# Kernel optimization log

Measured on AMD Instinct MI355X. Metric: run time of the kernel, lower is better.

Reference implementation:

```python
import jax, jax.numpy as jnp
import numpy as np

B, L, D, R = 16, 256, 1024, 128

def setup_inputs() -> dict:
    key = jax.random.key(0)
    k1, k2 = jax.random.split(key)
    batch = jax.random.normal(k1, (B, L, D), dtype=jnp.float32)
    # proj initialized uniform(-0.05, 0.05) in the original
    proj = jax.random.uniform(k2, (D, R), dtype=jnp.float32, minval=-0.05, maxval=0.05)
    return {"batch": batch, "proj": proj}

def reference(batch, proj):
    # [B, L, R] projected embeddings
    t = jnp.matmul(batch, proj)
    # all-pairs squared L2 distances: sum_r (t[b,i,r] - t[b,j,r])^2 -> [B, L, L]
    diffs = t[:, :, None, :] - t[:, None, :, :]  # [B, L, L, R]
    squared_distances = jnp.sum(diffs * diffs, axis=-1)
    return squared_distances
```

## Files before the change

### kernel.cpp

```cpp
#include <hip/hip_runtime.h>
#include <stdint.h>

#define B_ 16
#define L_ 256
#define D_ 1024
#define R_ 128
#define M_ (B_*L_)

typedef short short8 __attribute__((ext_vector_type(8)));
typedef float f32x4 __attribute__((ext_vector_type(4)));

__device__ __forceinline__ unsigned short f2bf(float f) {
  union { float f; unsigned int u; } v; v.f = f;
  unsigned int r = v.u + 0x7FFFu + ((v.u >> 16) & 1u);
  return (unsigned short)(r >> 16);
}
__device__ __forceinline__ float bf2f(unsigned short s) {
  union { unsigned int u; float f; } v; v.u = ((unsigned int)s) << 16;
  return v.f;
}
__device__ __forceinline__ void gload_lds16(const void* g, void* l) {
  __builtin_amdgcn_global_load_lds(
      (const __attribute__((address_space(1))) unsigned int*)g,
      (__attribute__((address_space(3))) unsigned int*)l, 16, 0, 0);
}

__global__ __launch_bounds__(256) void k0_transpose_cast(
    const float* __restrict__ P, unsigned short* __restrict__ PbT) {
  int id = blockIdx.x * 256 + threadIdx.x;
  int n  = id & 127;
  int kc = id >> 7;
  union { unsigned short s[8]; uint4 v; } u;
#pragma unroll
  for (int j = 0; j < 8; ++j) u.s[j] = f2bf(P[(kc * 8 + j) * R_ + n]);
  *reinterpret_cast<uint4*>(&PbT[(size_t)n * D_ + kc * 8]) = u.v;
}

__global__ __launch_bounds__(512) void k1_gemm(
    const float* __restrict__ X, const unsigned short* __restrict__ PbT,
    unsigned short* __restrict__ Tb, float* __restrict__ Nrm) {
  __shared__ unsigned short sX[2][16 * 128];
  __shared__ unsigned short sP[2][128 * 128];
  __shared__ float nacc[16][8];

  const int tid  = threadIdx.x;
  const int lane = tid & 63;
  const int w    = tid >> 6;
  const int m0   = blockIdx.x * 16;

  const int xr = tid >> 5;
  const int xk = (tid & 31) * 4;

  f32x4 acc;
  acc[0] = 0.f; acc[1] = 0.f; acc[2] = 0.f; acc[3] = 0.f;

  auto stage = [&](int buf, int kt) {
    const int k0 = kt * 128;
    float4 xv = *reinterpret_cast<const float4*>(&X[(size_t)(m0 + xr) * D_ + k0 + xk]);
    uint2 p;
    p.x = (unsigned int)f2bf(xv.x) | ((unsigned int)f2bf(xv.y) << 16);
    p.y = (unsigned int)f2bf(xv.z) | ((unsigned int)f2bf(xv.w) << 16);
    int byte_in_row = (xk * 2) ^ ((xr & 7) << 4);
    *reinterpret_cast<uint2*>(reinterpret_cast<char*>(&sX[buf][0]) + xr * 256 + byte_in_row) = p;
#pragma unroll
    for (int i = 0; i < 4; ++i) {
      int c = tid + 512 * i;
      int row = c >> 4, ch = c & 15;
      gload_lds16(&PbT[(size_t)row * D_ + k0 + ((ch ^ (row & 7)) * 8)],
                  reinterpret_cast<char*>(&sP[buf][0]) + c * 16);
    }
  };

  auto compute = [&](int buf) {
    const char* xb = reinterpret_cast<const char*>(&sX[buf][0]);
    const char* pb = reinterpret_cast<const char*>(&sP[buf][0]);
    const int nb = w * 16;
#pragma unroll
    for (int s = 0; s < 4; ++s) {
      int koffb = s * 64 + ((lane >> 4) << 4);
      int ar = lane & 15;
      short8 a = *reinterpret_cast<const short8*>(xb + ar * 256 + (koffb ^ ((ar & 7) << 4)));
      int br = nb + (lane & 15);
      short8 b = *reinterpret_cast<const short8*>(pb + br * 256 + (koffb ^ ((br & 7) << 4)));
      acc = __builtin_amdgcn_mfma_f32_16x16x32_bf16(a, b, acc, 0, 0, 0);
    }
  };

  stage(0, 0);
  __syncthreads();
  int buf = 0;
#pragma unroll
  for (int kt = 0; kt < 8; ++kt) {
    if (kt < 7) stage(buf ^ 1, kt + 1);
    compute(buf);
    __syncthreads();
    buf ^= 1;
  }

  const int nb = w * 16;
  const int col = lane & 15;
#pragma unroll
  for (int q = 0; q < 4; ++q) {
    int row = ((lane >> 4) << 2) + q;
    unsigned short hv = f2bf(acc[q]);
    Tb[(size_t)(m0 + row) * R_ + nb + col] = hv;
    float tr = bf2f(hv);
    float s = tr * tr;
    s += __shfl_xor(s, 1); s += __shfl_xor(s, 2);
    s += __shfl_xor(s, 4); s += __shfl_xor(s, 8);
    if (col == 0) nacc[row][w] = s;
  }
  __syncthreads();
  if (tid < 16) {
    float t = 0.f;
#pragma unroll
    for (int i = 0; i < 8; ++i) t += nacc[tid][i];
    Nrm[m0 + tid] = t;
  }
}

__global__ __launch_bounds__(256) void k2_gram(
    const unsigned short* __restrict__ Tb, const float* __restrict__ Nrm,
    float* __restrict__ Out) {
  __shared__ unsigned short sI[2 * 16 * 64];
  __shared__ unsigned short sJ[2 * 128 * 64];

  const int tid  = threadIdx.x;
  const int lane = tid & 63;
  const int w    = tid >> 6;
  const int blk  = blockIdx.x;
  const int b    = blk >> 5;
  const int it   = (blk >> 1) & 15;
  const int jh   = blk & 1;

  {
    int h = tid >> 7, row = (tid >> 3) & 15, ch = tid & 7;
    gload_lds16(&Tb[(size_t)(b * L_ + it * 16 + row) * R_ + h * 64 + ((ch ^ (row & 7)) * 8)],
                reinterpret_cast<char*>(sI) + tid * 16);
  }
#pragma unroll
  for (int i = 0; i < 8; ++i) {
    int c = tid + 256 * i;
    int h = c >> 10, row = (c >> 3) & 127, ch = c & 7;
    gload_lds16(&Tb[(size_t)(b * L_ + jh * 128 + row) * R_ + h * 64 + ((ch ^ (row & 7)) * 8)],
                reinterpret_cast<char*>(sJ) + c * 16);
  }
  __syncthreads();

  f32x4 acc[2];
#pragma unroll
  for (int ct = 0; ct < 2; ++ct) { acc[ct][0]=0.f; acc[ct][1]=0.f; acc[ct][2]=0.f; acc[ct][3]=0.f; }

  const char* ib = reinterpret_cast<const char*>(sI);
  const char* jb = reinterpret_cast<const char*>(sJ);
#pragma unroll
  for (int s = 0; s < 4; ++s) {
    int h = s >> 1;
    int col = (s & 1) * 64 + ((lane >> 4) << 4);
    int ar = lane & 15;
    short8 a = *reinterpret_cast<const short8*>(ib + h * 2048 + ar * 128 + (col ^ ((ar & 7) << 4)));
#pragma unroll
    for (int ct = 0; ct < 2; ++ct) {
      int br = w * 32 + ct * 16 + (lane & 15);
      short8 bv = *reinterpret_cast<const short8*>(jb + h * 16384 + br * 128 + (col ^ ((br & 7) << 4)));
      acc[ct] = __builtin_amdgcn_mfma_f32_16x16x32_bf16(a, bv, acc[ct], 0, 0, 0);
    }
  }

  const int col = lane & 15;
  float ni[4];
#pragma unroll
  for (int q = 0; q < 4; ++q)
    ni[q] = Nrm[b * L_ + it * 16 + ((lane >> 4) << 2) + q];
#pragma unroll
  for (int ct = 0; ct < 2; ++ct) {
    int j = jh * 128 + w * 32 + ct * 16 + col;
    float nj = Nrm[b * L_ + j];
#pragma unroll
    for (int q = 0; q < 4; ++q) {
      int il = it * 16 + ((lane >> 4) << 2) + q;
      float v = ni[q] + nj - 2.0f * acc[ct][q];
      Out[(size_t)(b * L_ + il) * L_ + j] = fmaxf(v, 0.0f);
    }
  }
}

extern "C" void kernel_launch(void* const* d_in, const int* in_sizes, int n_in,
                              void* d_out, int out_size, void* d_ws, size_t ws_size,
                              hipStream_t stream) {
  const float* X = (const float*)d_in[0];
  const float* P = (const float*)d_in[1];
  float* Out = (float*)d_out;
  char* ws = (char*)d_ws;
  unsigned short* PbT = (unsigned short*)ws;
  unsigned short* Tb  = (unsigned short*)(ws + (size_t)R_ * D_ * 2);
  float* Nrm = (float*)(ws + (size_t)R_ * D_ * 2 + (size_t)M_ * R_ * 2);

  k0_transpose_cast<<<64, 256, 0, stream>>>(P, PbT);
  k1_gemm<<<M_ / 16, 512, 0, stream>>>(X, PbT, Tb, Nrm);
  k2_gram<<<B_ * 16 * 2, 256, 0, stream>>>(Tb, Nrm, Out);
}
```

Baseline: 24.50 us.

## Split GEMM over N halves and compute norms inside the Gram kernel

The projection GEMM now launches twice as many 256-thread blocks, each computing a 64-column half of R, with a swizzled block order. The row-norm computation moves out of the GEMM into the Gram kernel, which recomputes norms from the LDS tiles. The Gram kernel also splits J into quarters, giving four times as many smaller blocks. This raises parallelism across CUs at the cost of loading X twice and computing norms redundantly in each Gram block.

After: 22.53 us. 1.09x faster.

```diff
diff --git a/kernel.cpp b/kernel.cpp
--- a/kernel.cpp
+++ b/kernel.cpp
@@ -36,37 +36,41 @@
   *reinterpret_cast<uint4*>(&PbT[(size_t)n * D_ + kc * 8]) = u.v;
 }
 
-__global__ __launch_bounds__(512) void k1_gemm(
+__global__ __launch_bounds__(256) void k1_gemm(
     const float* __restrict__ X, const unsigned short* __restrict__ PbT,
-    unsigned short* __restrict__ Tb, float* __restrict__ Nrm) {
+    unsigned short* __restrict__ Tb) {
   __shared__ unsigned short sX[2][16 * 128];
-  __shared__ unsigned short sP[2][128 * 128];
-  __shared__ float nacc[16][8];
+  __shared__ unsigned short sP[2][64 * 128];
 
   const int tid  = threadIdx.x;
   const int lane = tid & 63;
   const int w    = tid >> 6;
-  const int m0   = blockIdx.x * 16;
-
-  const int xr = tid >> 5;
-  const int xk = (tid & 31) * 4;
+  const int lb   = (blockIdx.x & 7) * 64 + (blockIdx.x >> 3);
+  const int m0   = (lb >> 1) * 16;
+  const int nb0  = (lb & 1) * 64;
 
   f32x4 acc;
   acc[0] = 0.f; acc[1] = 0.f; acc[2] = 0.f; acc[3] = 0.f;
 
   auto stage = [&](int buf, int kt) {
     const int k0 = kt * 128;
-    float4 xv = *reinterpret_cast<const float4*>(&X[(size_t)(m0 + xr) * D_ + k0 + xk]);
-    uint2 p;
-    p.x = (unsigned int)f2bf(xv.x) | ((unsigned int)f2bf(xv.y) << 16);
-    p.y = (unsigned int)f2bf(xv.z) | ((unsigned int)f2bf(xv.w) << 16);
-    int byte_in_row = (xk * 2) ^ ((xr & 7) << 4);
-    *reinterpret_cast<uint2*>(reinterpret_cast<char*>(&sX[buf][0]) + xr * 256 + byte_in_row) = p;
+#pragma unroll
+    for (int i = 0; i < 2; ++i) {
+      int c = tid + 256 * i;
+      int row = c >> 5;
+      int kq  = (c & 31) * 4;
+      float4 xv = *reinterpret_cast<const float4*>(&X[(size_t)(m0 + row) * D_ + k0 + kq]);
+      uint2 p;
+      p.x = (unsigned int)f2bf(xv.x) | ((unsigned int)f2bf(xv.y) << 16);
+      p.y = (unsigned int)f2bf(xv.z) | ((unsigned int)f2bf(xv.w) << 16);
+      int byte_in_row = (kq * 2) ^ ((row & 7) << 4);
+      *reinterpret_cast<uint2*>(reinterpret_cast<char*>(&sX[buf][0]) + row * 256 + byte_in_row) = p;
+    }
 #pragma unroll
     for (int i = 0; i < 4; ++i) {
-      int c = tid + 512 * i;
+      int c = tid + 256 * i;
       int row = c >> 4, ch = c & 15;
-      gload_lds16(&PbT[(size_t)row * D_ + k0 + ((ch ^ (row & 7)) * 8)],
+      gload_lds16(&PbT[(size_t)(nb0 + row) * D_ + k0 + ((ch ^ (row & 7)) * 8)],
                   reinterpret_cast<char*>(&sP[buf][0]) + c * 16);
     }
   };
@@ -74,13 +78,12 @@
   auto compute = [&](int buf) {
     const char* xb = reinterpret_cast<const char*>(&sX[buf][0]);
     const char* pb = reinterpret_cast<const char*>(&sP[buf][0]);
-    const int nb = w * 16;
 #pragma unroll
     for (int s = 0; s < 4; ++s) {
       int koffb = s * 64 + ((lane >> 4) << 4);
       int ar = lane & 15;
       short8 a = *reinterpret_cast<const short8*>(xb + ar * 256 + (koffb ^ ((ar & 7) << 4)));
-      int br = nb + (lane & 15);
+      int br = w * 16 + (lane & 15);
       short8 b = *reinterpret_cast<const short8*>(pb + br * 256 + (koffb ^ ((br & 7) << 4)));
       acc = __builtin_amdgcn_mfma_f32_16x16x32_bf16(a, b, acc, 0, 0, 0);
     }
@@ -97,91 +100,81 @@
     buf ^= 1;
   }
 
-  const int nb = w * 16;
   const int col = lane & 15;
 #pragma unroll
   for (int q = 0; q < 4; ++q) {
     int row = ((lane >> 4) << 2) + q;
-    unsigned short hv = f2bf(acc[q]);
-    Tb[(size_t)(m0 + row) * R_ + nb + col] = hv;
-    float tr = bf2f(hv);
-    float s = tr * tr;
-    s += __shfl_xor(s, 1); s += __shfl_xor(s, 2);
-    s += __shfl_xor(s, 4); s += __shfl_xor(s, 8);
-    if (col == 0) nacc[row][w] = s;
-  }
-  __syncthreads();
-  if (tid < 16) {
-    float t = 0.f;
-#pragma unroll
-    for (int i = 0; i < 8; ++i) t += nacc[tid][i];
-    Nrm[m0 + tid] = t;
+    Tb[(size_t)(m0 + row) * R_ + nb0 + w * 16 + col] = f2bf(acc[q]);
   }
 }
 
 __global__ __launch_bounds__(256) void k2_gram(
-    const unsigned short* __restrict__ Tb, const float* __restrict__ Nrm,
-    float* __restrict__ Out) {
-  __shared__ unsigned short sI[2 * 16 * 64];
-  __shared__ unsigned short sJ[2 * 128 * 64];
+    const unsigned short* __restrict__ Tb, float* __restrict__ Out) {
+  __shared__ unsigned short sI[16 * 128];
+  __shared__ unsigned short sJ[64 * 128];
+  __shared__ float nI[16], nJ[64];
 
   const int tid  = threadIdx.x;
   const int lane = tid & 63;
   const int w    = tid >> 6;
   const int blk  = blockIdx.x;
-  const int b    = blk >> 5;
-  const int it   = (blk >> 1) & 15;
-  const int jh   = blk & 1;
+  const int b    = blk >> 6;
+  const int it   = (blk >> 2) & 15;
+  const int jq   = blk & 3;
 
   {
-    int h = tid >> 7, row = (tid >> 3) & 15, ch = tid & 7;
-    gload_lds16(&Tb[(size_t)(b * L_ + it * 16 + row) * R_ + h * 64 + ((ch ^ (row & 7)) * 8)],
+    int row = tid >> 4, ch = tid & 15;
+    gload_lds16(&Tb[(size_t)(b * L_ + it * 16 + row) * R_ + ((ch ^ (row & 7)) * 8)],
                 reinterpret_cast<char*>(sI) + tid * 16);
   }
 #pragma unroll
-  for (int i = 0; i < 8; ++i) {
+  for (int i = 0; i < 4; ++i) {
     int c = tid + 256 * i;
-    int h = c >> 10, row = (c >> 3) & 127, ch = c & 7;
-    gload_lds16(&Tb[(size_t)(b * L_ + jh * 128 + row) * R_ + h * 64 + ((ch ^ (row & 7)) * 8)],
+    int row = c >> 4, ch = c & 15;
+    gload_lds16(&Tb[(size_t)(b * L_ + jq * 64 + row) * R_ + ((ch ^ (row & 7)) * 8)],
                 reinterpret_cast<char*>(sJ) + c * 16);
   }
   __syncthreads();
 
-  f32x4 acc[2];
+  if (tid < 160) {
+    int row = tid >> 1, h = tid & 1;
+    const char* base = (row < 16) ? reinterpret_cast<const char*>(sI)
+                                  : reinterpret_cast<const char*>(sJ);
+    int r = (row < 16) ? row : row - 16;
+    float s = 0.f;
 #pragma unroll
-  for (int ct = 0; ct < 2; ++ct) { acc[ct][0]=0.f; acc[ct][1]=0.f; acc[ct][2]=0.f; acc[ct][3]=0.f; }
+    for (int j = 0; j < 8; ++j) {
+      short8 v = *reinterpret_cast<const short8*>(base + r * 256 + ((h * 128 + j * 16) ^ ((r & 7) << 4)));
+#pragma unroll
+      for (int e = 0; e < 8; ++e) { float f = bf2f((unsigned short)v[e]); s += f * f; }
+    }
+    s += __shfl_xor(s, 1);
+    if (h == 0) { if (row < 16) nI[row] = s; else nJ[row - 16] = s; }
+  }
 
+  f32x4 acc;
+  acc[0] = 0.f; acc[1] = 0.f; acc[2] = 0.f; acc[3] = 0.f;
   const char* ib = reinterpret_cast<const char*>(sI);
   const char* jb = reinterpret_cast<const char*>(sJ);
 #pragma unroll
   for (int s = 0; s < 4; ++s) {
-    int h = s >> 1;
-    int col = (s & 1) * 64 + ((lane >> 4) << 4);
+    int koffb = s * 64 + ((lane >> 4) << 4);
     int ar = lane & 15;
-    short8 a = *reinterpret_cast<const short8*>(ib + h * 2048 + ar * 128 + (col ^ ((ar & 7) << 4)));
-#pragma unroll
-    for (int ct = 0; ct < 2; ++ct) {
-      int br = w * 32 + ct * 16 + (lane & 15);
-      short8 bv = *reinterpret_cast<const short8*>(jb + h * 16384 + br * 128 + (col ^ ((br & 7) << 4)));
-      acc[ct] = __builtin_amdgcn_mfma_f32_16x16x32_bf16(a, bv, acc[ct], 0, 0, 0);
-    }
+    short8 a = *reinterpret_cast<const short8*>(ib + ar * 256 + (koffb ^ ((ar & 7) << 4)));
+    int br = w * 16 + (lane & 15);
+    short8 bv = *reinterpret_cast<const short8*>(jb + br * 256 + (koffb ^ ((br & 7) << 4)));
+    acc = __builtin_amdgcn_mfma_f32_16x16x32_bf16(a, bv, acc, 0, 0, 0);
   }
+  __syncthreads();
 
   const int col = lane & 15;
-  float ni[4];
+  const int jj = w * 16 + col;
+  const float nj = nJ[jj];
 #pragma unroll
-  for (int q = 0; q < 4; ++q)
-    ni[q] = Nrm[b * L_ + it * 16 + ((lane >> 4) << 2) + q];
-#pragma unroll
-  for (int ct = 0; ct < 2; ++ct) {
-    int j = jh * 128 + w * 32 + ct * 16 + col;
-    float nj = Nrm[b * L_ + j];
-#pragma unroll
-    for (int q = 0; q < 4; ++q) {
-      int il = it * 16 + ((lane >> 4) << 2) + q;
-      float v = ni[q] + nj - 2.0f * acc[ct][q];
-      Out[(size_t)(b * L_ + il) * L_ + j] = fmaxf(v, 0.0f);
-    }
+  for (int q = 0; q < 4; ++q) {
+    int ir = ((lane >> 4) << 2) + q;
+    float v = nI[ir] + nj - 2.0f * acc[q];
+    Out[(size_t)(b * L_ + it * 16 + ir) * L_ + jq * 64 + jj] = fmaxf(v, 0.0f);
   }
 }
 
@@ -194,9 +187,8 @@
   char* ws = (char*)d_ws;
   unsigned short* PbT = (unsigned short*)ws;
   unsigned short* Tb  = (unsigned short*)(ws + (size_t)R_ * D_ * 2);
-  float* Nrm = (float*)(ws + (size_t)R_ * D_ * 2 + (size_t)M_ * R_ * 2);
 
   k0_transpose_cast<<<64, 256, 0, stream>>>(P, PbT);
-  k1_gemm<<<M_ / 16, 512, 0, stream>>>(X, PbT, Tb, Nrm);
-  k2_gram<<<B_ * 16 * 2, 256, 0, stream>>>(Tb, Nrm, Out);
+  k1_gemm<<<M_ / 16 * 2, 256, 0, stream>>>(X, PbT, Tb);
+  k2_gram<<<B_ * 16 * 4, 256, 0, stream>>>(Tb, Out);
 }
```
